# Optimization experiments

Hardware: AMD Instinct MI355X
Metric: run time of the kernel (lower is better)

Reference implementation:

```python
import jax, jax.numpy as jnp
import numpy as np

N = 200000
D = 256  # node_dim

def setup_inputs() -> dict:
    key = jax.random.key(0)
    k0, k1, kw, kb = jax.random.split(key, 4)
    var_v0 = jax.random.normal(k0, (N, D), dtype=jnp.float32)
    var_v1 = jax.random.normal(k1, (N, D), dtype=jnp.float32)
    W = jax.random.normal(kw, (2 * D, 2 * D), dtype=jnp.float32) * 0.02
    b = jax.random.normal(kb, (2 * D,), dtype=jnp.float32) * 0.02
    return {"var_v0": var_v0, "var_v1": var_v1, "W": W, "b": b}

def reference(var_v0, var_v1, W, b):
    # cat along feature dim -> [N, 2D]
    catted = jnp.concatenate([var_v0, var_v1], axis=1)
    # Linear (torch convention: x @ W.T + b) then ReLU
    activated = jax.nn.relu(catted @ W.T + b)
    # sum-pool over all nodes -> [1, 2D] (replaces the python loop of adds)
    readout = jnp.sum(activated, axis=0, keepdims=True)
    return readout
```

## Files before the change

kernel.cpp:

```cpp
#include <hip/hip_runtime.h>
#include <hip/hip_bf16.h>


typedef __bf16 bf16x8 __attribute__((ext_vector_type(8)));
typedef float  f32x4  __attribute__((ext_vector_type(4)));
typedef unsigned short u16x4 __attribute__((ext_vector_type(4)));

#define BM 128
#define BN 128
#define BK 32
#define NK 16
#define SLOTS 128
#define NCB 4

static __device__ __forceinline__ int swz(int r) { return (r & 3) ^ ((r >> 2) & 3); }
static __device__ __forceinline__ unsigned short f2bf(float f) {
    return __builtin_bit_cast(unsigned short, (__bf16)f);
}
static __device__ __forceinline__ bf16x8 pack8(float4 a, float4 b) {
    bf16x8 o;
    o[0] = (__bf16)a.x; o[1] = (__bf16)a.y; o[2] = (__bf16)a.z; o[3] = (__bf16)a.w;
    o[4] = (__bf16)b.x; o[5] = (__bf16)b.y; o[6] = (__bf16)b.z; o[7] = (__bf16)b.w;
    return o;
}

#define GLDS16(G, L) __builtin_amdgcn_global_load_lds(                       \
    (const __attribute__((address_space(1))) void*)(G),                     \
    (__attribute__((address_space(3))) void*)(L), 16, 0, 0)

__global__ void conv_w_bf16(const float* __restrict__ W, unsigned short* __restrict__ Wb) {
    int idx = (blockIdx.x * blockDim.x + threadIdx.x) * 4;
    float4 f = *(const float4*)(W + idx);
    u16x4 p;
    p[0] = f2bf(f.x); p[1] = f2bf(f.y); p[2] = f2bf(f.z); p[3] = f2bf(f.w);
    *(u16x4*)(Wb + idx) = p;
}

template<bool WBF16>
__global__ __launch_bounds__(256) void fused_gemm_pool(
    const float* __restrict__ v0, const float* __restrict__ v1,
    const float* __restrict__ Wf, const unsigned short* __restrict__ Wb,
    const float* __restrict__ b,
    float* __restrict__ partial, int N, int numRB)
{
    __shared__ unsigned short As[2][BM * BK];
    __shared__ unsigned short Bs[2][BN * BK];
    __shared__ float ldsPart[4][64];

    int bid   = blockIdx.x;
    int group = bid >> 5;
    int xcd   = bid & 7;
    int cb    = (bid >> 3) & 3;
    int slot  = group * 8 + xcd;

    int tid = threadIdx.x, wid = tid >> 6, lane = tid & 63;
    int wr = wid >> 1, wc = wid & 1, l15 = lane & 15, l4 = lane >> 4;

    int rowA[2], offAg[2], offAw[2], offBg[2], offBw[2], offBgl[2];
    #pragma unroll
    for (int i = 0; i < 2; ++i) {
        int m = tid + i * 256;
        int r = m >> 2, c = m & 3;
        rowA[i]  = r;
        offAg[i] = r * 256 + c * 8;
        offAw[i] = r * BK + ((c ^ swz(r)) * 8);
        offBg[i] = (cb * 128 + r) * 512 + c * 8;
        offBw[i] = offAw[i];
        int mu = (wid + i * 4) * 64 + lane;
        int br = mu >> 2, bc = mu & 3;
        offBgl[i] = (cb * 128 + br) * 512 + ((bc ^ swz(br)) * 8);
    }
    int offAf[4], offBf[4];
    #pragma unroll
    for (int f = 0; f < 4; ++f) {
        int r = wr * 64 + f * 16 + l15;
        offAf[f] = r * BK + ((l4 ^ swz(r)) * 8);
        int cc = wc * 64 + f * 16 + l15;
        offBf[f] = cc * BK + ((l4 ^ swz(cc)) * 8);
    }

    float bv[4];
    #pragma unroll
    for (int nf = 0; nf < 4; ++nf) bv[nf] = b[cb * 128 + wc * 64 + nf * 16 + l15];

    float csum[4] = {0.f, 0.f, 0.f, 0.f};
    float4 rA[2][4];
    float4 rB[2][4];

    for (int rbk = slot; rbk < numRB; rbk += SLOTS) {
        int rowBase = rbk * BM;

        f32x4 acc[4][4];
        #pragma unroll
        for (int mf = 0; mf < 4; ++mf)
            #pragma unroll
            for (int nf = 0; nf < 4; ++nf)
                acc[mf][nf] = (f32x4){0.f, 0.f, 0.f, 0.f};

        auto loadA = [&](int kt, int s) {
            const float* src = (kt < 8) ? v0 : v1;
            int k0 = (kt & 7) * 32;
            #pragma unroll
            for (int i = 0; i < 2; ++i) {
                float4 f0 = {0,0,0,0}, f1 = {0,0,0,0};
                if (rowBase + rowA[i] < N) {
                    const float* p = src + (size_t)rowBase * 256 + offAg[i] + k0;
                    f0 = *(const float4*)p;
                    f1 = *(const float4*)(p + 4);
                }
                rA[s][i * 2]     = f0;
                rA[s][i * 2 + 1] = f1;
            }
        };
        auto writeA = [&](int s, int buf) {
            #pragma unroll
            for (int i = 0; i < 2; ++i)
                *(bf16x8*)&As[buf][offAw[i]] = pack8(rA[s][i * 2], rA[s][i * 2 + 1]);
        };
        auto stageBglds = [&](int kt, int buf) {
            int k0 = kt * 32;
            #pragma unroll
            for (int j = 0; j < 2; ++j)
                GLDS16(Wb + offBgl[j] + k0, &Bs[buf][(wid + j * 4) * 512]);
        };
        auto loadB = [&](int kt, int s) {
            int k0 = kt * 32;
            #pragma unroll
            for (int i = 0; i < 2; ++i) {
                const float* p = Wf + offBg[i] + k0;
                rB[s][i * 2]     = *(const float4*)p;
                rB[s][i * 2 + 1] = *(const float4*)(p + 4);
            }
        };
        auto writeB = [&](int s, int buf) {
            #pragma unroll
            for (int i = 0; i < 2; ++i)
                *(bf16x8*)&Bs[buf][offBw[i]] = pack8(rB[s][i * 2], rB[s][i * 2 + 1]);
        };

        if constexpr (WBF16) stageBglds(0, 0); else loadB(0, 0);
        loadA(0, 0);
        loadA(1, 1);
        if constexpr (!WBF16) loadB(1, 1);
        writeA(0, 0);
        if constexpr (!WBF16) writeB(0, 0);

        #pragma unroll
        for (int kt = 0; kt < NK; ++kt) {
            int cur = kt & 1;
            __syncthreads();
            if constexpr (WBF16) {
                if (kt + 1 < NK) stageBglds(kt + 1, cur ^ 1);
            }
            if (kt + 2 < NK) {
                loadA(kt + 2, cur);
                if constexpr (!WBF16) loadB(kt + 2, cur);
            }
            bf16x8 af[4], bf[4];
            #pragma unroll
            for (int f = 0; f < 4; ++f) af[f] = *(const bf16x8*)&As[cur][offAf[f]];
            #pragma unroll
            for (int f = 0; f < 4; ++f) bf[f] = *(const bf16x8*)&Bs[cur][offBf[f]];
            #pragma unroll
            for (int mf = 0; mf < 4; ++mf)
                #pragma unroll
                for (int nf = 0; nf < 4; ++nf)
                    acc[mf][nf] = __builtin_amdgcn_mfma_f32_16x16x32_bf16(
                        af[mf], bf[nf], acc[mf][nf], 0, 0, 0);
            if (kt + 1 < NK) {
                writeA(cur ^ 1, cur ^ 1);
                if constexpr (!WBF16) writeB(cur ^ 1, cur ^ 1);
            }
        }

        #pragma unroll
        for (int nf = 0; nf < 4; ++nf) {
            float bb = bv[nf];
            #pragma unroll
            for (int mf = 0; mf < 4; ++mf) {
                int rbase = rowBase + wr * 64 + mf * 16 + l4 * 4;
                #pragma unroll
                for (int r = 0; r < 4; ++r) {
                    float v = fmaxf(acc[mf][nf][r] + bb, 0.f);
                    if (rbase + r < N) csum[nf] += v;
                }
            }
        }
    }

    #pragma unroll
    for (int nf = 0; nf < 4; ++nf) {
        float s = csum[nf];
        s += __shfl_xor(s, 16);
        s += __shfl_xor(s, 32);
        if (lane < 16) ldsPart[wid][nf * 16 + lane] = s;
    }
    __syncthreads();
    if (tid < 128) {
        int half = tid >> 6, c = tid & 63;
        float v = ldsPart[half][c] + ldsPart[half + 2][c];
        partial[(size_t)slot * 512 + cb * 128 + tid] = v;
    }
}

__global__ void reduce_partials(const float* __restrict__ partial, float* __restrict__ out)
{
    int c = blockIdx.x * blockDim.x + threadIdx.x;
    if (c < 512) {
        float s = 0.f;
        for (int s2 = 0; s2 < SLOTS; ++s2) s += partial[(size_t)s2 * 512 + c];
        out[c] = s;
    }
}

extern "C" void kernel_launch(void* const* d_in, const int* in_sizes, int n_in,
                              void* d_out, int out_size, void* d_ws, size_t ws_size,
                              hipStream_t stream)
{
    const float* v0 = (const float*)d_in[0];
    const float* v1 = (const float*)d_in[1];
    const float* Wf = (const float*)d_in[2];
    const float* b  = (const float*)d_in[3];
    float* out      = (float*)d_out;

    int N = in_sizes[0] / 256;
    int numRB = (N + BM - 1) / BM;

    size_t wbytes = (size_t)512 * 512 * sizeof(unsigned short);
    size_t pbytes = (size_t)SLOTS * 512 * sizeof(float);

    if (ws_size >= wbytes + pbytes) {
        unsigned short* Wb = (unsigned short*)d_ws;
        float* partial = (float*)((char*)d_ws + wbytes);
        conv_w_bf16<<<dim3(256), dim3(256), 0, stream>>>(Wf, Wb);
        fused_gemm_pool<true><<<dim3(SLOTS * NCB), dim3(256), 0, stream>>>(
            v0, v1, Wf, Wb, b, partial, N, numRB);
        reduce_partials<<<dim3(2), dim3(256), 0, stream>>>(partial, out);
    } else {
        float* partial = (float*)d_ws;
        fused_gemm_pool<false><<<dim3(SLOTS * NCB), dim3(256), 0, stream>>>(
            v0, v1, Wf, nullptr, b, partial, N, numRB);
        reduce_partials<<<dim3(2), dim3(256), 0, stream>>>(partial, out);
    }
}
```

Baseline: 247.3 us.

## Halve row tile to 64 and raise grid slots to 512 for occupancy

```diff
diff --git a/kernel.cpp b/kernel.cpp
--- a/kernel.cpp
+++ b/kernel.cpp
@@ -6,12 +6,10 @@
 typedef float  f32x4  __attribute__((ext_vector_type(4)));
 typedef unsigned short u16x4 __attribute__((ext_vector_type(4)));
 
-#define BM 128
+#define BM 64
 #define BN 128
 #define BK 32
 #define NK 16
-#define SLOTS 128
-#define NCB 4
 
 static __device__ __forceinline__ int swz(int r) { return (r & 3) ^ ((r >> 2) & 3); }
 static __device__ __forceinline__ unsigned short f2bf(float f) {
@@ -41,11 +39,11 @@
     const float* __restrict__ v0, const float* __restrict__ v1,
     const float* __restrict__ Wf, const unsigned short* __restrict__ Wb,
     const float* __restrict__ b,
-    float* __restrict__ partial, int N, int numRB)
+    float* __restrict__ partial, int N, int numRB, int slots)
 {
     __shared__ unsigned short As[2][BM * BK];
     __shared__ unsigned short Bs[2][BN * BK];
-    __shared__ float ldsPart[4][64];
+    __shared__ float ldsPart[2][128];
 
     int bid   = blockIdx.x;
     int group = bid >> 5;
@@ -56,25 +54,27 @@
     int tid = threadIdx.x, wid = tid >> 6, lane = tid & 63;
     int wr = wid >> 1, wc = wid & 1, l15 = lane & 15, l4 = lane >> 4;
 
-    int rowA[2], offAg[2], offAw[2], offBg[2], offBw[2], offBgl[2];
-    #pragma unroll
-    for (int i = 0; i < 2; ++i) {
-        int m = tid + i * 256;
-        int r = m >> 2, c = m & 3;
-        rowA[i]  = r;
-        offAg[i] = r * 256 + c * 8;
-        offAw[i] = r * BK + ((c ^ swz(r)) * 8);
-        offBg[i] = (cb * 128 + r) * 512 + c * 8;
-        offBw[i] = offAw[i];
-        int mu = (wid + i * 4) * 64 + lane;
+    int rowA = tid >> 2, colA = tid & 3;
+    int offAg = rowA * 256 + colA * 8;
+    int offAw = rowA * BK + ((colA ^ swz(rowA)) * 8);
+
+    int offBgl[2], offBg[2], offBw[2];
+    #pragma unroll
+    for (int j = 0; j < 2; ++j) {
+        int mu = (wid + j * 4) * 64 + lane;
         int br = mu >> 2, bc = mu & 3;
-        offBgl[i] = (cb * 128 + br) * 512 + ((bc ^ swz(br)) * 8);
-    }
-    int offAf[4], offBf[4];
+        offBgl[j] = (cb * 128 + br) * 512 + ((bc ^ swz(br)) * 8);
+        offBg[j]  = (cb * 128 + br) * 512 + bc * 8;
+        offBw[j]  = br * BK + ((bc ^ swz(br)) * 8);
+    }
+    int offAf[2], offBf[4];
+    #pragma unroll
+    for (int f = 0; f < 2; ++f) {
+        int r = wr * 32 + f * 16 + l15;
+        offAf[f] = r * BK + ((l4 ^ swz(r)) * 8);
+    }
     #pragma unroll
     for (int f = 0; f < 4; ++f) {
-        int r = wr * 64 + f * 16 + l15;
-        offAf[f] = r * BK + ((l4 ^ swz(r)) * 8);
         int cc = wc * 64 + f * 16 + l15;
         offBf[f] = cc * BK + ((l4 ^ swz(cc)) * 8);
     }
@@ -84,15 +84,15 @@
     for (int nf = 0; nf < 4; ++nf) bv[nf] = b[cb * 128 + wc * 64 + nf * 16 + l15];
 
     float csum[4] = {0.f, 0.f, 0.f, 0.f};
-    float4 rA[2][4];
+    float4 rA[2][2];
     float4 rB[2][4];
 
-    for (int rbk = slot; rbk < numRB; rbk += SLOTS) {
+    for (int rbk = slot; rbk < numRB; rbk += slots) {
         int rowBase = rbk * BM;
 
-        f32x4 acc[4][4];
+        f32x4 acc[2][4];
         #pragma unroll
-        for (int mf = 0; mf < 4; ++mf)
+        for (int mf = 0; mf < 2; ++mf)
             #pragma unroll
             for (int nf = 0; nf < 4; ++nf)
                 acc[mf][nf] = (f32x4){0.f, 0.f, 0.f, 0.f};
@@ -100,22 +100,16 @@
         auto loadA = [&](int kt, int s) {
             const float* src = (kt < 8) ? v0 : v1;
             int k0 = (kt & 7) * 32;
-            #pragma unroll
-            for (int i = 0; i < 2; ++i) {
-                float4 f0 = {0,0,0,0}, f1 = {0,0,0,0};
-                if (rowBase + rowA[i] < N) {
-                    const float* p = src + (size_t)rowBase * 256 + offAg[i] + k0;
-                    f0 = *(const float4*)p;
-                    f1 = *(const float4*)(p + 4);
-                }
-                rA[s][i * 2]     = f0;
-                rA[s][i * 2 + 1] = f1;
-            }
+            float4 f0 = {0,0,0,0}, f1 = {0,0,0,0};
+            if (rowBase + rowA < N) {
+                const float* p = src + (size_t)rowBase * 256 + offAg + k0;
+                f0 = *(const float4*)p;
+                f1 = *(const float4*)(p + 4);
+            }
+            rA[s][0] = f0; rA[s][1] = f1;
         };
         auto writeA = [&](int s, int buf) {
-            #pragma unroll
-            for (int i = 0; i < 2; ++i)
-                *(bf16x8*)&As[buf][offAw[i]] = pack8(rA[s][i * 2], rA[s][i * 2 + 1]);
+            *(bf16x8*)&As[buf][offAw] = pack8(rA[s][0], rA[s][1]);
         };
         auto stageBglds = [&](int kt, int buf) {
             int k0 = kt * 32;
@@ -126,16 +120,16 @@
         auto loadB = [&](int kt, int s) {
             int k0 = kt * 32;
             #pragma unroll
-            for (int i = 0; i < 2; ++i) {
-                const float* p = Wf + offBg[i] + k0;
-                rB[s][i * 2]     = *(const float4*)p;
-                rB[s][i * 2 + 1] = *(const float4*)(p + 4);
+            for (int j = 0; j < 2; ++j) {
+                const float* p = Wf + offBg[j] + k0;
+                rB[s][j * 2]     = *(const float4*)p;
+                rB[s][j * 2 + 1] = *(const float4*)(p + 4);
             }
         };
         auto writeB = [&](int s, int buf) {
             #pragma unroll
-            for (int i = 0; i < 2; ++i)
-                *(bf16x8*)&Bs[buf][offBw[i]] = pack8(rB[s][i * 2], rB[s][i * 2 + 1]);
+            for (int j = 0; j < 2; ++j)
+                *(bf16x8*)&Bs[buf][offBw[j]] = pack8(rB[s][j * 2], rB[s][j * 2 + 1]);
         };
 
         if constexpr (WBF16) stageBglds(0, 0); else loadB(0, 0);
@@ -156,13 +150,13 @@
                 loadA(kt + 2, cur);
                 if constexpr (!WBF16) loadB(kt + 2, cur);
             }
-            bf16x8 af[4], bf[4];
-            #pragma unroll
-            for (int f = 0; f < 4; ++f) af[f] = *(const bf16x8*)&As[cur][offAf[f]];
+            bf16x8 af[2], bf[4];
+            #pragma unroll
+            for (int f = 0; f < 2; ++f) af[f] = *(const bf16x8*)&As[cur][offAf[f]];
             #pragma unroll
             for (int f = 0; f < 4; ++f) bf[f] = *(const bf16x8*)&Bs[cur][offBf[f]];
             #pragma unroll
-            for (int mf = 0; mf < 4; ++mf)
+            for (int mf = 0; mf < 2; ++mf)
                 #pragma unroll
                 for (int nf = 0; nf < 4; ++nf)
                     acc[mf][nf] = __builtin_amdgcn_mfma_f32_16x16x32_bf16(
@@ -177,8 +171,8 @@
         for (int nf = 0; nf < 4; ++nf) {
             float bb = bv[nf];
             #pragma unroll
-            for (int mf = 0; mf < 4; ++mf) {
-                int rbase = rowBase + wr * 64 + mf * 16 + l4 * 4;
+            for (int mf = 0; mf < 2; ++mf) {
+                int rbase = rowBase + wr * 32 + mf * 16 + l4 * 4;
                 #pragma unroll
                 for (int r = 0; r < 4; ++r) {
                     float v = fmaxf(acc[mf][nf][r] + bb, 0.f);
@@ -193,22 +187,20 @@
         float s = csum[nf];
         s += __shfl_xor(s, 16);
         s += __shfl_xor(s, 32);
-        if (lane < 16) ldsPart[wid][nf * 16 + lane] = s;
+        if (lane < 16) ldsPart[wr][wc * 64 + nf * 16 + lane] = s;
     }
     __syncthreads();
-    if (tid < 128) {
-        int half = tid >> 6, c = tid & 63;
-        float v = ldsPart[half][c] + ldsPart[half + 2][c];
-        partial[(size_t)slot * 512 + cb * 128 + tid] = v;
-    }
-}
-
-__global__ void reduce_partials(const float* __restrict__ partial, float* __restrict__ out)
+    if (tid < 128)
+        partial[(size_t)slot * 512 + cb * 128 + tid] = ldsPart[0][tid] + ldsPart[1][tid];
+}
+
+__global__ void reduce_partials(const float* __restrict__ partial,
+                                float* __restrict__ out, int slots)
 {
-    int c = blockIdx.x * blockDim.x + threadIdx.x;
+    int c = threadIdx.x;
     if (c < 512) {
         float s = 0.f;
-        for (int s2 = 0; s2 < SLOTS; ++s2) s += partial[(size_t)s2 * 512 + c];
+        for (int i = 0; i < slots; ++i) s += partial[(size_t)i * 512 + c];
         out[c] = s;
     }
 }
@@ -226,20 +218,27 @@
     int N = in_sizes[0] / 256;
     int numRB = (N + BM - 1) / BM;
 
-    size_t wbytes = (size_t)512 * 512 * sizeof(unsigned short);
-    size_t pbytes = (size_t)SLOTS * 512 * sizeof(float);
-
-    if (ws_size >= wbytes + pbytes) {
+    const size_t wbytes = (size_t)512 * 512 * sizeof(unsigned short);
+    auto pbytes = [](int s) { return (size_t)s * 512 * sizeof(float); };
+
+    int slots; bool useWb;
+    if      (ws_size >= wbytes + pbytes(512)) { slots = 512; useWb = true;  }
+    else if (ws_size >= wbytes + pbytes(256)) { slots = 256; useWb = true;  }
+    else if (ws_size >= pbytes(512))          { slots = 512; useWb = false; }
+    else if (ws_size >= pbytes(256))          { slots = 256; useWb = false; }
+    else                                      { slots = 128; useWb = false; }
+
+    if (useWb) {
         unsigned short* Wb = (unsigned short*)d_ws;
         float* partial = (float*)((char*)d_ws + wbytes);
         conv_w_bf16<<<dim3(256), dim3(256), 0, stream>>>(Wf, Wb);
-        fused_gemm_pool<true><<<dim3(SLOTS * NCB), dim3(256), 0, stream>>>(
-            v0, v1, Wf, Wb, b, partial, N, numRB);
-        reduce_partials<<<dim3(2), dim3(256), 0, stream>>>(partial, out);
+        fused_gemm_pool<true><<<dim3(slots * 4), dim3(256), 0, stream>>>(
+            v0, v1, Wf, Wb, b, partial, N, numRB, slots);
+        reduce_partials<<<dim3(1), dim3(512), 0, stream>>>(partial, out, slots);
     } else {
         float* partial = (float*)d_ws;
-        fused_gemm_pool<false><<<dim3(SLOTS * NCB), dim3(256), 0, stream>>>(
-            v0, v1, Wf, nullptr, b, partial, N, numRB);
-        reduce_partials<<<dim3(2), dim3(256), 0, stream>>>(partial, out);
-    }
-}
+        fused_gemm_pool<false><<<dim3(slots * 4), dim3(256), 0, stream>>>(
+            v0, v1, Wf, nullptr, b, partial, N, numRB, slots);
+        reduce_partials<<<dim3(1), dim3(512), 0, stream>>>(partial, out, slots);
+    }
+}
```

Result: slower. 459.7 us (+85.9%).
